# Kernel tuning notes

Measured on AMD Instinct MI355X. Metric: run time of the kernel, lower is better.

Reference implementation:

```python
import jax, jax.numpy as jnp
import numpy as np

B = 4096          # effective_batch_size (world_size=1)
D = 128           # embedding_dim
T = 0.5           # temperature
CW = 0.5          # confidence_weight
PT = 0.8          # positive_threshold (cosine)


def setup_inputs() -> dict:
    key = jax.random.key(0)
    emb = jax.random.normal(key, (B, D), dtype=jnp.float32)
    emb = emb / jnp.linalg.norm(emb, axis=1, keepdims=True)  # cosine-sim embeddings
    return {"embedding": emb}


def reference(embedding):
    b = embedding.shape[0]
    half = b // 2
    idx = jnp.arange(b)
    pos_idx = (idx + half) % b  # positive pair index (other augmented view)

    # exp(sim / T), [B, B]
    sim = jnp.exp(embedding @ embedding.T / T)

    # precomputed masks (world_size=1, rank=0, num_pos=2):
    # positive mask: the other view; negative mask: everything except self and its pair
    pos_mask = jnp.zeros((b, b), dtype=sim.dtype).at[idx, pos_idx].set(1.0)
    neg_mask = 1.0 - pos_mask - jnp.eye(b, dtype=sim.dtype)

    all_pos = sim * pos_mask
    all_neg = sim * neg_mask

    pos_sim = sim[idx, pos_idx]  # [B]

    # diff_sim: |sim - pos_sim| on upper triangle (j >= i), 3 elsewhere,
    # with diagonal and (i, i+half) for i < half also set to 3
    upper = idx[None, :] >= idx[:, None]
    excl = jnp.eye(b, dtype=bool) | ((idx[:, None] < half) & (idx[None, :] == idx[:, None] + half))
    diff_sim = jnp.where(upper & ~excl, jnp.abs(sim - pos_sim[:, None]), jnp.asarray(3.0, sim.dtype))

    # all argmin locations (torch.where(diff_sim == min)) -> boolean select mask
    min_mask = diff_sim == jnp.min(diff_sim)
    conf = (jnp.log(pos_sim) * T >= PT)[:, None]  # per-anchor confidence gate
    sel = min_mask & conf

    # false-negative reweighting (pos read of all_neg happens before neg update)
    new_pos = jnp.where(sel & (all_pos == 0.0), CW * all_neg, all_pos)
    new_neg = jnp.where(sel & (all_neg != 0.0), (1.0 - CW) * all_neg, all_neg)

    pos = jnp.sum(new_pos, axis=1)
    neg = jnp.sum(new_neg, axis=1)
    return -jnp.mean(jnp.log(pos / (pos + neg)))
```

## Files before the change

kernel.cpp:

```cpp
#include <hip/hip_runtime.h>
#include <hip/hip_bf16.h>
#include <math.h>

#define B_N  4096
#define HALF 2048
#define D_K  128
#define BT   128
#define NBT  32

typedef __attribute__((ext_vector_type(8))) short bf16x8;
typedef __attribute__((ext_vector_type(4))) float f32x4;

__device__ __forceinline__ void stage_tile_cvt(const float* __restrict__ emb,
                                               int row0, ushort* lds) {
    int t = threadIdx.x;
    const float4* src = (const float4*)(emb + (size_t)row0 * D_K);
    char* dst = (char*)lds;
#pragma unroll
    for (int it = 0; it < 8; ++it) {
        int f = t + 256 * it;
        int r = f >> 4;
        int c = f & 15;
        float4 v0 = src[r * 32 + c * 2];
        float4 v1 = src[r * 32 + c * 2 + 1];
        union { __hip_bfloat162 h; unsigned u; } c0, c1, c2, c3;
        c0.h = __float22bfloat162_rn(make_float2(v0.x, v0.y));
        c1.h = __float22bfloat162_rn(make_float2(v0.z, v0.w));
        c2.h = __float22bfloat162_rn(make_float2(v1.x, v1.y));
        c3.h = __float22bfloat162_rn(make_float2(v1.z, v1.w));
        uint4 w = {c0.u, c1.u, c2.u, c3.u};
        int byte = (r << 8) | (((c ^ (r & 7)) & 15) << 4);
        *(uint4*)(dst + byte) = w;
    }
}

__device__ __forceinline__ bf16x8 read_frag(const ushort* lds, int row, int kbyte) {
    int byte = ((row << 8) | kbyte) ^ ((row & 7) << 4);
    return *(const bf16x8*)((const char*)lds + byte);
}

__device__ __forceinline__ void tile_mfma_sw(const ushort* Al, const ushort* Bl,
                                             int lane, int wr, f32x4 acc[2][8]) {
#pragma unroll
    for (int m = 0; m < 2; ++m)
#pragma unroll
        for (int n = 0; n < 8; ++n) acc[m][n] = (f32x4){0.f, 0.f, 0.f, 0.f};

    int rA = wr * 32 + (lane & 15);
    int rB = (lane & 15);
    int kb0 = (lane >> 4) << 4;
#pragma unroll
    for (int ks = 0; ks < 4; ++ks) {
        int kb = ks * 64 + kb0;
        bf16x8 a[2], b[8];
#pragma unroll
        for (int m = 0; m < 2; ++m) a[m] = read_frag(Al, rA + m * 16, kb);
#pragma unroll
        for (int n = 0; n < 8; ++n) b[n] = read_frag(Bl, rB + n * 16, kb);
#pragma unroll
        for (int m = 0; m < 2; ++m)
#pragma unroll
            for (int n = 0; n < 8; ++n)
                acc[m][n] = __builtin_amdgcn_mfma_f32_16x16x32_bf16(
                    b[n], a[m], acc[m][n], 0, 0, 0);
    }
}

__global__ __launch_bounds__(256) void k0_prep(const float* __restrict__ emb,
                                               float* __restrict__ pos_sim,
                                               float* __restrict__ conf,
                                               unsigned* __restrict__ minbits,
                                               unsigned* __restrict__ counter) {
    int i = blockIdx.x * 256 + threadIdx.x;
    int p = i ^ HALF;
    const float4* a = (const float4*)(emb + (size_t)i * D_K);
    const float4* b = (const float4*)(emb + (size_t)p * D_K);
    float acc = 0.f;
#pragma unroll
    for (int k = 0; k < D_K / 4; ++k) {
        float4 av = a[k], bv = b[k];
        acc = fmaf(av.x, bv.x, acc);
        acc = fmaf(av.y, bv.y, acc);
        acc = fmaf(av.z, bv.z, acc);
        acc = fmaf(av.w, bv.w, acc);
    }
    float ps = expf(acc * 2.0f);
    pos_sim[i] = ps;
    conf[i]    = (logf(ps) * 0.5f >= 0.8f) ? 1.0f : 0.0f;
    if (i == 0) { *minbits = __float_as_uint(3.0f); *counter = 0u; }
}

__global__ __launch_bounds__(256, 2) void k1_main(const float* __restrict__ emb,
                                                  const float* __restrict__ pos_sim,
                                                  const float* __restrict__ conf,
                                                  float* __restrict__ negpart,
                                                  float* __restrict__ corrpart,
                                                  unsigned* __restrict__ block_min,
                                                  unsigned* __restrict__ minbits) {
    int bi = blockIdx.y, bj = blockIdx.x;
    __shared__ ushort Al[BT * D_K];
    __shared__ ushort Bl[BT * D_K];
    stage_tile_cvt(emb, bi * BT, Al);
    stage_tile_cvt(emb, bj * BT, Bl);
    __syncthreads();

    int tid = threadIdx.x, lane = tid & 63, wr = tid >> 6;
    f32x4 acc[2][8];
    tile_mfma_sw(Al, Bl, lane, wr, acc);

#pragma unroll
    for (int m = 0; m < 2; ++m)
#pragma unroll
        for (int n = 0; n < 8; ++n)
#pragma unroll
            for (int reg = 0; reg < 4; ++reg)
                acc[m][n][reg] = __expf(acc[m][n][reg] * 2.0f);

    int ib = bi * BT + wr * 32 + (lane & 15);
    int jb = bj * BT + ((lane >> 4) << 2);
    bool diag = (bi == bj), post = (bj == (bi ^ 16)), up = (bj > bi);

    float lmin = 3.0f;
    float psi_[2];
#pragma unroll
    for (int m = 0; m < 2; ++m) {
        int i = ib + m * 16;
        float psi = pos_sim[i];
        psi_[m] = psi;
        int pidx = i ^ HALF;
        float negp = 0.f;
        if (!diag && !post) {
#pragma unroll
            for (int n = 0; n < 8; ++n)
#pragma unroll
                for (int reg = 0; reg < 4; ++reg) {
                    float s = acc[m][n][reg];
                    negp += s;
                    if (up) lmin = fminf(lmin, fabsf(s - psi));
                }
        } else if (diag) {
#pragma unroll
            for (int n = 0; n < 8; ++n)
#pragma unroll
                for (int reg = 0; reg < 4; ++reg) {
                    float s = acc[m][n][reg];
                    int j = jb + n * 16 + reg;
                    if (j != i) negp += s;
                    if (j > i) lmin = fminf(lmin, fabsf(s - psi));
                }
        } else {
#pragma unroll
            for (int n = 0; n < 8; ++n)
#pragma unroll
                for (int reg = 0; reg < 4; ++reg) {
                    float s = acc[m][n][reg];
                    int j = jb + n * 16 + reg;
                    if (j != pidx) {
                        negp += s;
                        if (up) lmin = fminf(lmin, fabsf(s - psi));
                    }
                }
        }
        negp += __shfl_xor(negp, 16);
        negp += __shfl_xor(negp, 32);
        if (lane < 16) negpart[bj * B_N + i] = negp;
    }

#pragma unroll
    for (int off = 32; off; off >>= 1)
        lmin = fminf(lmin, __shfl_xor(lmin, off));
    __shared__ float wred[4];
    if (lane == 0) wred[wr] = lmin;
    __syncthreads();
    float bmin = fminf(fminf(wred[0], wred[1]), fminf(wred[2], wred[3]));
    if (tid == 0) {
        block_min[bi * NBT + bj] = __float_as_uint(bmin);
        atomicMin(minbits, __float_as_uint(bmin));
    }

    float corr_[2] = {0.f, 0.f};
    bool anyc = (conf[ib] != 0.f) || (conf[ib + 16] != 0.f);
    if (__any(anyc)) {
#pragma unroll
        for (int m = 0; m < 2; ++m) {
            int i = ib + m * 16;
            float psi = psi_[m];
            int pidx = i ^ HALF;
            bool ci = (conf[i] != 0.f);
            float corr = 0.f;
#pragma unroll
            for (int n = 0; n < 8; ++n)
#pragma unroll
                for (int reg = 0; reg < 4; ++reg) {
                    float s = acc[m][n][reg];
                    int j = jb + n * 16 + reg;
                    bool valid = (j > i) && !(j == pidx && i < HALF);
                    float d = valid ? fabsf(s - psi) : 3.0f;
                    if (ci && d == bmin && j != i && j != pidx)
                        corr += 0.5f * s;
                }
            corr += __shfl_xor(corr, 16);
            corr += __shfl_xor(corr, 32);
            corr_[m] = corr;
        }
    }
    if (lane < 16) {
        corrpart[bj * B_N + ib]      = corr_[0];
        corrpart[bj * B_N + ib + 16] = corr_[1];
    }
}

__global__ __launch_bounds__(128) void k3_loss(const float* __restrict__ pos_sim,
                                               const float* __restrict__ negpart,
                                               const float* __restrict__ corrpart,
                                               const unsigned* __restrict__ block_min,
                                               const unsigned* __restrict__ minbits,
                                               float* __restrict__ partial,
                                               unsigned* __restrict__ counter,
                                               float* __restrict__ out) {
    int bi = blockIdx.x, t = threadIdx.x;
    int i = bi * 128 + t;
    unsigned gm = *minbits;
    float neg = 0.f, corr = 0.f;
#pragma unroll
    for (int bj = 0; bj < NBT; ++bj) {
        neg += negpart[bj * B_N + i];
        if (block_min[bi * NBT + bj] == gm)
            corr += corrpart[bj * B_N + i];
    }
    float pos = pos_sim[i] + corr;
    float ng  = neg - corr;
    float l = logf(pos / (pos + ng));
#pragma unroll
    for (int off = 32; off; off >>= 1) l += __shfl_xor(l, off);
    __shared__ float w2[2];
    if ((t & 63) == 0) w2[t >> 6] = l;
    __syncthreads();
    if (t == 0) {
        partial[bi] = w2[0] + w2[1];
        __threadfence();
        unsigned c = atomicAdd(counter, 1u);
        if (c == NBT - 1) {
            __threadfence();
            float tot = 0.f;
            volatile float* vp = partial;
            for (int b = 0; b < NBT; ++b) tot += vp[b];
            *out = -tot / (float)B_N;
        }
    }
}

extern "C" void kernel_launch(void* const* d_in, const int* in_sizes, int n_in,
                              void* d_out, int out_size, void* d_ws, size_t ws_size,
                              hipStream_t stream) {
    const float* emb = (const float*)d_in[0];
    float* out = (float*)d_out;

    float* fbase = (float*)d_ws;
    float*    pos_sim   = fbase;
    float*    conf      = fbase + 4096;
    float*    negpart   = fbase + 8192;
    float*    corrpart  = negpart + NBT * B_N;
    float*    partial   = corrpart + NBT * B_N;
    unsigned* block_min = (unsigned*)(partial + 32);
    unsigned* minbits   = block_min + 1024;
    unsigned* counter   = minbits + 1;

    k0_prep<<<16, 256, 0, stream>>>(emb, pos_sim, conf, minbits, counter);
    dim3 grid(NBT, NBT);
    k1_main<<<grid, 256, 0, stream>>>(emb, pos_sim, conf, negpart, corrpart,
                                      block_min, minbits);
    k3_loss<<<NBT, 128, 0, stream>>>(pos_sim, negpart, corrpart, block_min,
                                     minbits, partial, counter, out);
}
```

Before: 38.97 us.

## Exploit Gram matrix symmetry: compute only upper-triangular tiles with atomic row/column sums

The main kernel now launches only the upper-triangular tile pairs (528 instead of 1024) and uses the symmetry of the similarity matrix. Each off-diagonal tile adds its row sums and, through shuffle-reduced column sums, its column sums into a shared per-row negative accumulator with atomics. Diagonal tiles reuse the A tile in LDS instead of staging B. The prep kernel is also split across 16 lanes per row for more parallelism. The cost is extra cross-lane shuffles and many float atomics, which also make the summation order nondeterministic.

After: 40.59 us. 1.04x slower.

```diff
diff --git a/kernel.cpp b/kernel.cpp
--- a/kernel.cpp
+++ b/kernel.cpp
@@ -7,6 +7,7 @@
 #define D_K  128
 #define BT   128
 #define NBT  32
+#define NBLK (NBT * (NBT + 1) / 2)
 
 typedef __attribute__((ext_vector_type(8))) short bf16x8;
 typedef __attribute__((ext_vector_type(4))) float f32x4;
@@ -69,44 +70,58 @@
 __global__ __launch_bounds__(256) void k0_prep(const float* __restrict__ emb,
                                                float* __restrict__ pos_sim,
                                                float* __restrict__ conf,
+                                               float* __restrict__ neg_acc,
                                                unsigned* __restrict__ minbits,
                                                unsigned* __restrict__ counter) {
-    int i = blockIdx.x * 256 + threadIdx.x;
-    int p = i ^ HALF;
-    const float4* a = (const float4*)(emb + (size_t)i * D_K);
-    const float4* b = (const float4*)(emb + (size_t)p * D_K);
-    float acc = 0.f;
-#pragma unroll
-    for (int k = 0; k < D_K / 4; ++k) {
-        float4 av = a[k], bv = b[k];
-        acc = fmaf(av.x, bv.x, acc);
-        acc = fmaf(av.y, bv.y, acc);
-        acc = fmaf(av.z, bv.z, acc);
-        acc = fmaf(av.w, bv.w, acc);
-    }
-    float ps = expf(acc * 2.0f);
-    pos_sim[i] = ps;
-    conf[i]    = (logf(ps) * 0.5f >= 0.8f) ? 1.0f : 0.0f;
-    if (i == 0) { *minbits = __float_as_uint(3.0f); *counter = 0u; }
+    int tid = threadIdx.x;
+    int r   = blockIdx.x * 16 + (tid >> 4);
+    int l16 = tid & 15;
+    const float* a = emb + (size_t)r * D_K + l16 * 8;
+    const float* b = emb + (size_t)(r ^ HALF) * D_K + l16 * 8;
+    float4 x0 = *(const float4*)a,       x1 = *(const float4*)(a + 4);
+    float4 y0 = *(const float4*)b,       y1 = *(const float4*)(b + 4);
+    float d = 0.f;
+    d = fmaf(x0.x, y0.x, d); d = fmaf(x0.y, y0.y, d);
+    d = fmaf(x0.z, y0.z, d); d = fmaf(x0.w, y0.w, d);
+    d = fmaf(x1.x, y1.x, d); d = fmaf(x1.y, y1.y, d);
+    d = fmaf(x1.z, y1.z, d); d = fmaf(x1.w, y1.w, d);
+#pragma unroll
+    for (int off = 1; off < 16; off <<= 1) d += __shfl_xor(d, off);
+    if (l16 == 0) {
+        float ps = expf(d * 2.0f);
+        pos_sim[r] = ps;
+        conf[r]    = (logf(ps) * 0.5f >= 0.8f) ? 1.0f : 0.0f;
+        neg_acc[r] = 0.f;
+    }
+    if (blockIdx.x == 0 && tid == 0) {
+        *minbits = __float_as_uint(3.0f);
+        *counter = 0u;
+    }
 }
 
 __global__ __launch_bounds__(256, 2) void k1_main(const float* __restrict__ emb,
                                                   const float* __restrict__ pos_sim,
                                                   const float* __restrict__ conf,
-                                                  float* __restrict__ negpart,
+                                                  float* __restrict__ neg_acc,
                                                   float* __restrict__ corrpart,
                                                   unsigned* __restrict__ block_min,
                                                   unsigned* __restrict__ minbits) {
-    int bi = blockIdx.y, bj = blockIdx.x;
+    int t = blockIdx.x, bi = 0;
+    while (t >= NBT - bi) { t -= NBT - bi; ++bi; }
+    int bj = bi + t;
+    bool diag = (bi == bj);
+    bool post = (bj == (bi ^ 16));
+
     __shared__ ushort Al[BT * D_K];
     __shared__ ushort Bl[BT * D_K];
     stage_tile_cvt(emb, bi * BT, Al);
-    stage_tile_cvt(emb, bj * BT, Bl);
+    if (!diag) stage_tile_cvt(emb, bj * BT, Bl);
     __syncthreads();
+    const ushort* Bs = diag ? Al : Bl;
 
     int tid = threadIdx.x, lane = tid & 63, wr = tid >> 6;
     f32x4 acc[2][8];
-    tile_mfma_sw(Al, Bl, lane, wr, acc);
+    tile_mfma_sw(Al, Bs, lane, wr, acc);
 
 #pragma unroll
     for (int m = 0; m < 2; ++m)
@@ -118,26 +133,26 @@
 
     int ib = bi * BT + wr * 32 + (lane & 15);
     int jb = bj * BT + ((lane >> 4) << 2);
-    bool diag = (bi == bj), post = (bj == (bi ^ 16)), up = (bj > bi);
-
+
+    float psi_[2];
     float lmin = 3.0f;
-    float psi_[2];
 #pragma unroll
     for (int m = 0; m < 2; ++m) {
         int i = ib + m * 16;
         float psi = pos_sim[i];
         psi_[m] = psi;
         int pidx = i ^ HALF;
-        float negp = 0.f;
+        float np0 = 0.f, np1 = 0.f, np2 = 0.f, np3 = 0.f;
+        float l0 = 3.f, l1 = 3.f, l2 = 3.f, l3 = 3.f;
         if (!diag && !post) {
 #pragma unroll
-            for (int n = 0; n < 8; ++n)
-#pragma unroll
-                for (int reg = 0; reg < 4; ++reg) {
-                    float s = acc[m][n][reg];
-                    negp += s;
-                    if (up) lmin = fminf(lmin, fabsf(s - psi));
-                }
+            for (int n = 0; n < 8; ++n) {
+                float s0 = acc[m][n][0], s1 = acc[m][n][1];
+                float s2 = acc[m][n][2], s3 = acc[m][n][3];
+                np0 += s0; np1 += s1; np2 += s2; np3 += s3;
+                l0 = fminf(l0, fabsf(s0 - psi)); l1 = fminf(l1, fabsf(s1 - psi));
+                l2 = fminf(l2, fabsf(s2 - psi)); l3 = fminf(l3, fabsf(s3 - psi));
+            }
         } else if (diag) {
 #pragma unroll
             for (int n = 0; n < 8; ++n)
@@ -145,8 +160,8 @@
                 for (int reg = 0; reg < 4; ++reg) {
                     float s = acc[m][n][reg];
                     int j = jb + n * 16 + reg;
-                    if (j != i) negp += s;
-                    if (j > i) lmin = fminf(lmin, fabsf(s - psi));
+                    if (j != i) np0 += s;
+                    if (j > i)  l0 = fminf(l0, fabsf(s - psi));
                 }
         } else {
 #pragma unroll
@@ -156,14 +171,42 @@
                     float s = acc[m][n][reg];
                     int j = jb + n * 16 + reg;
                     if (j != pidx) {
-                        negp += s;
-                        if (up) lmin = fminf(lmin, fabsf(s - psi));
+                        np0 += s;
+                        l0 = fminf(l0, fabsf(s - psi));
                     }
                 }
         }
+        float negp = (np0 + np1) + (np2 + np3);
         negp += __shfl_xor(negp, 16);
         negp += __shfl_xor(negp, 32);
-        if (lane < 16) negpart[bj * B_N + i] = negp;
+        if (lane < 16) atomicAdd(&neg_acc[i], negp);
+        lmin = fminf(lmin, fminf(fminf(l0, l1), fminf(l2, l3)));
+    }
+
+    if (!diag) {
+        float colc[32];
+#pragma unroll
+        for (int n = 0; n < 8; ++n)
+#pragma unroll
+            for (int reg = 0; reg < 4; ++reg) {
+                float s0 = acc[0][n][reg], s1 = acc[1][n][reg];
+                if (post) {
+                    int j = jb + n * 16 + reg;
+                    if (j == (ib ^ HALF))        s0 = 0.f;
+                    if (j == ((ib + 16) ^ HALF)) s1 = 0.f;
+                }
+                colc[n * 4 + reg] = s0 + s1;
+            }
+#pragma unroll
+        for (int off = 1; off < 16; off <<= 1)
+#pragma unroll
+            for (int v = 0; v < 32; ++v)
+                colc[v] += __shfl_xor(colc[v], off);
+        if ((lane & 15) == 0) {
+#pragma unroll
+            for (int v = 0; v < 32; ++v)
+                atomicAdd(&neg_acc[jb + (v >> 2) * 16 + (v & 3)], colc[v]);
+        }
     }
 
 #pragma unroll
@@ -194,10 +237,9 @@
                 for (int reg = 0; reg < 4; ++reg) {
                     float s = acc[m][n][reg];
                     int j = jb + n * 16 + reg;
-                    bool valid = (j > i) && !(j == pidx && i < HALF);
+                    bool valid = diag ? (j > i) : (post ? (j != pidx) : true);
                     float d = valid ? fabsf(s - psi) : 3.0f;
-                    if (ci && d == bmin && j != i && j != pidx)
-                        corr += 0.5f * s;
+                    if (ci && d == bmin) corr += 0.5f * s;
                 }
             corr += __shfl_xor(corr, 16);
             corr += __shfl_xor(corr, 32);
@@ -211,7 +253,7 @@
 }
 
 __global__ __launch_bounds__(128) void k3_loss(const float* __restrict__ pos_sim,
-                                               const float* __restrict__ negpart,
+                                               const float* __restrict__ neg_acc,
                                                const float* __restrict__ corrpart,
                                                const unsigned* __restrict__ block_min,
                                                const unsigned* __restrict__ minbits,
@@ -221,16 +263,12 @@
     int bi = blockIdx.x, t = threadIdx.x;
     int i = bi * 128 + t;
     unsigned gm = *minbits;
-    float neg = 0.f, corr = 0.f;
-#pragma unroll
-    for (int bj = 0; bj < NBT; ++bj) {
-        neg += negpart[bj * B_N + i];
-        if (block_min[bi * NBT + bj] == gm)
-            corr += corrpart[bj * B_N + i];
-    }
+    float corr = 0.f;
+    for (int bj = bi; bj < NBT; ++bj)
+        if (block_min[bi * NBT + bj] == gm) corr += corrpart[bj * B_N + i];
+    float neg = neg_acc[i] - corr;
     float pos = pos_sim[i] + corr;
-    float ng  = neg - corr;
-    float l = logf(pos / (pos + ng));
+    float l = logf(pos / (pos + neg));
 #pragma unroll
     for (int off = 32; off; off >>= 1) l += __shfl_xor(l, off);
     __shared__ float w2[2];
@@ -239,7 +277,7 @@
     if (t == 0) {
         partial[bi] = w2[0] + w2[1];
         __threadfence();
-        unsigned c = atomicAdd(counter, 1u);
+        unsigned c = atomicAdd((unsigned*)counter, 1u);
         if (c == NBT - 1) {
             __threadfence();
             float tot = 0.f;
@@ -259,17 +297,16 @@
     float* fbase = (float*)d_ws;
     float*    pos_sim   = fbase;
     float*    conf      = fbase + 4096;
-    float*    negpart   = fbase + 8192;
-    float*    corrpart  = negpart + NBT * B_N;
+    float*    neg_acc   = fbase + 8192;
+    float*    corrpart  = fbase + 12288;
     float*    partial   = corrpart + NBT * B_N;
     unsigned* block_min = (unsigned*)(partial + 32);
     unsigned* minbits   = block_min + 1024;
     unsigned* counter   = minbits + 1;
 
-    k0_prep<<<16, 256, 0, stream>>>(emb, pos_sim, conf, minbits, counter);
-    dim3 grid(NBT, NBT);
-    k1_main<<<grid, 256, 0, stream>>>(emb, pos_sim, conf, negpart, corrpart,
+    k0_prep<<<256, 256, 0, stream>>>(emb, pos_sim, conf, neg_acc, minbits, counter);
+    k1_main<<<NBLK, 256, 0, stream>>>(emb, pos_sim, conf, neg_acc, corrpart,
                                       block_min, minbits);
-    k3_loss<<<NBT, 128, 0, stream>>>(pos_sim, negpart, corrpart, block_min,
+    k3_loss<<<NBT, 128, 0, stream>>>(pos_sim, neg_acc, corrpart, block_min,
                                      minbits, partial, counter, out);
 }
```
